# Kernel tuning notes

Measured on AMD Instinct MI355X. Metric: run time of the kernel, lower is better.

The kernel has to match this reference:

```python
import jax, jax.numpy as jnp
import numpy as np
import math

B, H, W, CV = 8, 128, 128, 256
T, CT = 77, 512
HEADS, HEAD_DIM = 8, 32
TOP_M = 5
LN_EPS = 1e-5
NORM_EPS = 1e-6
CLAMP = 2.0


def _ln(x, w, b):
    mu = jnp.mean(x, axis=-1, keepdims=True)
    var = jnp.mean(jnp.square(x - mu), axis=-1, keepdims=True)
    return (x - mu) * jax.lax.rsqrt(var + LN_EPS) * w + b


def _l2norm(x):
    n = jnp.sqrt(jnp.sum(jnp.square(x), axis=-1, keepdims=True))
    return x / jnp.maximum(n, NORM_EPS)


def setup_inputs() -> dict:
    key = jax.random.key(0)
    ks = jax.random.split(key, 12)
    s = 0.02
    return {
        "visual_features": jax.random.normal(ks[0], (B, H, W, CV), jnp.float32),
        "text_features": jax.random.normal(ks[1], (B, T, CT), jnp.float32),
        "norm1_w": jnp.ones((CV,), jnp.float32),
        "norm1_b": jnp.zeros((CV,), jnp.float32),
        "q_w": s * jax.random.normal(ks[2], (CV, CV), jnp.float32),
        "q_b": jnp.zeros((CV,), jnp.float32),
        "k_w": s * jax.random.normal(ks[3], (CT, CV), jnp.float32),
        "k_b": jnp.zeros((CV,), jnp.float32),
        "v_w": s * jax.random.normal(ks[4], (CT, CV), jnp.float32),
        "v_b": jnp.zeros((CV,), jnp.float32),
        "out_w": s * jax.random.normal(ks[5], (CV, CV), jnp.float32),
        "out_b": jnp.zeros((CV,), jnp.float32),
        "gate_w": s * jax.random.normal(ks[6], (CV, 1), jnp.float32),
        "gate_b": jnp.zeros((1,), jnp.float32),
        "logit_scale": jnp.asarray(math.log(1.0 / 0.07), jnp.float32),
        "alpha": jnp.asarray(0.1, jnp.float32),
        "norm2_w": jnp.ones((CV,), jnp.float32),
        "norm2_b": jnp.zeros((CV,), jnp.float32),
        "ffn1_w": s * jax.random.normal(ks[7], (CV, 4 * CV), jnp.float32),
        "ffn1_b": jnp.zeros((4 * CV,), jnp.float32),
        "ffn2_w": s * jax.random.normal(ks[8], (4 * CV, CV), jnp.float32),
        "ffn2_b": jnp.zeros((CV,), jnp.float32),
    }


def reference(visual_features, text_features, norm1_w, norm1_b, q_w, q_b, k_w, k_b,
              v_w, v_b, out_w, out_b, gate_w, gate_b, logit_scale, alpha,
              norm2_w, norm2_b, ffn1_w, ffn1_b, ffn2_w, ffn2_b):
    b, h, w, cv = visual_features.shape
    n = h * w
    # Pre-LN then flatten spatial dims: (B, N, Cv)
    x = _ln(visual_features, norm1_w, norm1_b).reshape(b, n, cv)
    q_full = x @ q_w + q_b                      # (B, N, Cv)
    k_full = text_features @ k_w + k_b          # (B, T, Cv)
    v_full = text_features @ v_w + v_b          # (B, T, Cv)
    # padding mask: all-zero text tokens
    pad = jnp.sum(jnp.abs(text_features), axis=-1) <= 1e-6  # (B, T)
    # cosine-normalize over FULL Cv dim, then split heads
    q = _l2norm(q_full).reshape(b, n, HEADS, HEAD_DIM)
    k = _l2norm(k_full).reshape(b, -1, HEADS, HEAD_DIM)
    v = v_full.reshape(b, -1, HEADS, HEAD_DIM)
    scale = jnp.exp(jnp.clip(logit_scale, -CLAMP, CLAMP)) / jnp.sqrt(jnp.float32(HEAD_DIM))
    sim = jnp.einsum('bnhd,bthd->bnht', q, k) * scale  # (B, N, Hh, T)
    sim = jnp.where(pad[:, None, None, :], -jnp.inf, sim)
    # top-k pruning over text tokens (threshold at k-th value; ties measure-zero)
    topv = jax.lax.top_k(sim, TOP_M)[0]
    sim = jnp.where(sim >= topv[..., -1:], sim, -jnp.inf)
    attn = jax.nn.softmax(sim, axis=-1)
    aligned = jnp.einsum('bnht,bthd->bnhd', attn, v).reshape(b, n, cv)
    aligned = aligned @ out_w + out_b
    gate = jax.nn.sigmoid(x @ gate_w + gate_b)  # (B, N, 1)
    y = x + alpha * gate * aligned
    y = _ln(y, norm2_w, norm2_b)
    ffn = jax.nn.gelu(y @ ffn1_w + ffn1_b, approximate=False) @ ffn2_w + ffn2_b
    y = y + ffn
    return y.reshape(b, h, w, cv)
```

## Files before the change

### kernel.cpp

```cpp
#include <hip/hip_runtime.h>
#include <hip/hip_bf16.h>

typedef _Float16 h16;
typedef __attribute__((ext_vector_type(8))) _Float16 halfx8;
typedef __attribute__((ext_vector_type(4))) _Float16 halfx4;
typedef __attribute__((ext_vector_type(4))) float f32x4;

__device__ __forceinline__ void gload_lds16(const void* g, void* l) {
  __builtin_amdgcn_global_load_lds((const __attribute__((address_space(1))) unsigned int*)g,
                                   (__attribute__((address_space(3))) unsigned int*)l, 16, 0, 0);
}
__device__ __forceinline__ unsigned umax_(unsigned a, unsigned b) { return a > b ? a : b; }
__device__ __forceinline__ unsigned umin_(unsigned a, unsigned b) { return a < b ? a : b; }

__device__ __forceinline__ float fast_gelu(float v) {
  float x2 = v * v;
  float w_ = v * fmaf(x2, 0.0713548163f, 1.5957691216f);
  float e = __expf(w_);
  float r = 1.f / (1.f + e);
  return v * e * r;
}

__global__ __launch_bounds__(256) void conv_all_kernel(
    const float* __restrict__ qw, const float* __restrict__ ow,
    const float* __restrict__ f1w, const float* __restrict__ f2w,
    h16* __restrict__ qwT, h16* __restrict__ owT,
    h16* __restrict__ f1T, h16* __restrict__ f2T)
{
  int bid = blockIdx.x, tid = threadIdx.x;
  const float* in; h16* out; int logN, K, base;
  if (bid < 256)       { in = qw;  out = qwT; logN = 8;  K = 256;  base = 0; }
  else if (bid < 512)  { in = ow;  out = owT; logN = 8;  K = 256;  base = 256; }
  else if (bid < 1536) { in = f1w; out = f1T; logN = 10; K = 256;  base = 512; }
  else                 { in = f2w; out = f2T; logN = 8;  K = 1024; base = 1536; }
  int idx = (bid - base) * 256 + tid;
  int k = idx >> logN, n = idx & ((1 << logN) - 1);
  out[(size_t)n * K + k] = (h16)in[idx];
}

__global__ __launch_bounds__(256) void text_kv_kernel(const float* __restrict__ tf,
    const float* __restrict__ kw, const float* __restrict__ kb,
    const float* __restrict__ vw, const float* __restrict__ vb,
    const float* __restrict__ lsp,
    h16* __restrict__ ko, h16* __restrict__ vo, float* __restrict__ padf)
{
  __shared__ h16 st[4 * 512];
  __shared__ float kro[4 * 256];
  __shared__ float ssc[4];
  int bx = blockIdx.x, b = bx / 20, tg = bx % 20, t0 = tg * 4;
  int tid = threadIdx.x, lane = tid & 63, wid = tid >> 6;
  for (int i = tid; i < 4 * 512; i += 256) {
    int tl = i >> 9, j = i & 511, t = t0 + tl;
    float v = (t < 77) ? tf[((size_t)b * 77 + t) * 512 + j] : 0.f;
    st[i] = (h16)v;
  }
  __syncthreads();
  {
    int t = t0 + wid;
    float a = 0.f;
    #pragma unroll
    for (int j = 0; j < 8; j++) a += fabsf((float)st[wid * 512 + lane + j * 64]);
    #pragma unroll
    for (int o = 32; o; o >>= 1) a += __shfl_xor(a, o);
    if (lane == 0) padf[b * 80 + t] = (a <= 1e-6f) ? -1e30f : 0.f;
  }
  int c = tid;
  float kacc[4], vacc[4];
  #pragma unroll
  for (int tl = 0; tl < 4; tl++) { kacc[tl] = kb[c]; vacc[tl] = vb[c]; }
  for (int j = 0; j < 512; j++) {
    float wkv = kw[(size_t)j * 256 + c];
    float wvv = vw[(size_t)j * 256 + c];
    #pragma unroll
    for (int tl = 0; tl < 4; tl++) {
      float x = (float)st[tl * 512 + j];
      kacc[tl] += x * wkv; vacc[tl] += x * wvv;
    }
  }
  #pragma unroll
  for (int tl = 0; tl < 4; tl++) kro[tl * 256 + c] = kacc[tl] * kacc[tl];
  __syncthreads();
  {
    float s2 = kro[wid * 256 + lane] + kro[wid * 256 + lane + 64]
             + kro[wid * 256 + lane + 128] + kro[wid * 256 + lane + 192];
    #pragma unroll
    for (int o = 32; o; o >>= 1) s2 += __shfl_xor(s2, o);
    if (lane == 0) {
      float ls = lsp[0];
      float scale = __expf(fminf(fmaxf(ls, -2.f), 2.f)) * rsqrtf(32.f);
      ssc[wid] = scale / fmaxf(sqrtf(s2), 1e-6f);
    }
  }
  __syncthreads();
  int h = c >> 5, d = c & 31, g = d >> 3, e = d & 7;
  #pragma unroll
  for (int tl = 0; tl < 4; tl++) {
    int t = t0 + tl;
    int kt = t >> 4, l15 = t & 15, ln = g * 16 + l15;
    size_t koff = ((((size_t)(b * 8 + h) * 5 + kt) * 64) + ln) * 8 + e;
    size_t voff = (((size_t)(b * 8 + h) * 80) + t) * 32 + d;
    ko[koff] = (t < 77) ? (h16)(kacc[tl] * ssc[tl]) : (h16)0.f;
    vo[voff] = (t < 77) ? (h16)vacc[tl] : (h16)0.f;
  }
}

__global__ __launch_bounds__(256) void ln1_kernel(const float* __restrict__ vis,
    const float* __restrict__ w, const float* __restrict__ bia,
    const float* __restrict__ gw, const float* __restrict__ gb,
    h16* __restrict__ x, float* __restrict__ gate)
{
  int lane = threadIdx.x & 63;
  size_t row = (size_t)blockIdx.x * 4 + (threadIdx.x >> 6);
  const float4 v = ((const float4*)(vis + row * 256))[lane];
  float s = v.x + v.y + v.z + v.w;
  float q = v.x * v.x + v.y * v.y + v.z * v.z + v.w * v.w;
  #pragma unroll
  for (int o = 32; o; o >>= 1) { s += __shfl_xor(s, o); q += __shfl_xor(q, o); }
  float mean = s * (1.f / 256.f);
  float rstd = rsqrtf(q * (1.f / 256.f) - mean * mean + 1e-5f);
  float4 wv = ((const float4*)w)[lane], bv = ((const float4*)bia)[lane];
  float x0 = (v.x - mean) * rstd * wv.x + bv.x;
  float x1 = (v.y - mean) * rstd * wv.y + bv.y;
  float x2 = (v.z - mean) * rstd * wv.z + bv.z;
  float x3 = (v.w - mean) * rstd * wv.w + bv.w;
  float4 gv = ((const float4*)gw)[lane];
  float g = x0 * gv.x + x1 * gv.y + x2 * gv.z + x3 * gv.w;
  #pragma unroll
  for (int o = 32; o; o >>= 1) g += __shfl_xor(g, o);
  if (lane == 0) gate[row] = 1.f / (1.f + __expf(-(g + gb[0])));
  halfx4 o4; o4[0] = (h16)x0; o4[1] = (h16)x1; o4[2] = (h16)x2; o4[3] = (h16)x3;
  ((halfx4*)(x + row * 256))[lane] = o4;
}

__global__ __launch_bounds__(256) void gemmQA_kernel(const h16* __restrict__ A,
    const h16* __restrict__ Wt, const float* __restrict__ bias,
    const h16* __restrict__ kk,
    const h16* __restrict__ vv,
    const float* __restrict__ padf,
    h16* __restrict__ outp)
{
  __shared__ char sA[8192];
  __shared__ char sB[32768];
  int m0 = blockIdx.x * 64;
  int tid = threadIdx.x, lane = tid & 63, wid = tid >> 6;
  int wn = wid;
  int l15 = lane & 15, l4 = lane >> 4, xk = l15 & 7;
  f32x4 acc[4][4];
  #pragma unroll
  for (int a = 0; a < 4; a++)
    #pragma unroll
    for (int b2 = 0; b2 < 4; b2++) acc[a][b2] = (f32x4){0.f, 0.f, 0.f, 0.f};
  const size_t sa = 512;
  int srow = lane >> 3;
  int scol = ((lane & 7) ^ srow) * 16;
  const char* Ab = (const char*)A + (size_t)m0 * sa + scol;
  const char* Bb = (const char*)Wt + scol;
  for (int k0 = 0; k0 < 256; k0 += 64) {
    #pragma unroll
    for (int cc = 0; cc < 2; cc++) {
      int ch = wid * 2 + cc;
      gload_lds16(Ab + (size_t)(ch * 8 + srow) * sa + k0 * 2, sA + ch * 1024);
    }
    #pragma unroll
    for (int cc = 0; cc < 8; cc++) {
      int ch = wid * 8 + cc;
      gload_lds16(Bb + (size_t)(ch * 8 + srow) * sa + k0 * 2, sB + ch * 1024);
    }
    asm volatile("s_waitcnt vmcnt(0)" ::: "memory");
    __syncthreads();
    #pragma unroll
    for (int ks = 0; ks < 2; ks++) {
      halfx8 af[4], bf[4];
      #pragma unroll
      for (int f = 0; f < 4; f++) {
        af[f] = *(const halfx8*)(sA + (f * 16 + l15) * 128 + (((ks * 4 + l4) ^ xk) * 16));
        bf[f] = *(const halfx8*)(sB + (wn * 64 + f * 16 + l15) * 128 + (((ks * 4 + l4) ^ xk) * 16));
      }
      #pragma unroll
      for (int fm = 0; fm < 4; fm++)
        #pragma unroll
        for (int fn = 0; fn < 4; fn++)
          acc[fm][fn] = __builtin_amdgcn_mfma_f32_16x16x32_f16(af[fm], bf[fn], acc[fm][fn], 0, 0, 0);
    }
    __syncthreads();
  }
  float bv[4];
  #pragma unroll
  for (int fn = 0; fn < 4; fn++) bv[fn] = bias[wn * 64 + fn * 16 + l15];
  float ps[4][4];
  #pragma unroll
  for (int fm = 0; fm < 4; fm++)
    #pragma unroll
    for (int r = 0; r < 4; r++) {
      float s = 0.f;
      #pragma unroll
      for (int fn = 0; fn < 4; fn++) {
        float v = acc[fm][fn][r] + bv[fn];
        acc[fm][fn][r] = v;
        s += v * v;
      }
      ps[fm][r] = s;
    }
  #pragma unroll
  for (int o = 1; o <= 8; o <<= 1)
    #pragma unroll
    for (int fm = 0; fm < 4; fm++)
      #pragma unroll
      for (int r = 0; r < 4; r++) ps[fm][r] += __shfl_xor(ps[fm][r], o);
  if (l15 == 0) {
    #pragma unroll
    for (int fm = 0; fm < 4; fm++)
      #pragma unroll
      for (int r = 0; r < 4; r++)
        ((float*)sA)[(fm * 16 + l4 * 4 + r) * 4 + wn] = ps[fm][r];
  }
  __syncthreads();
  #pragma unroll
  for (int fm = 0; fm < 4; fm++)
    #pragma unroll
    for (int r = 0; r < 4; r++) {
      const float* p = (const float*)sA + (fm * 16 + l4 * 4 + r) * 4;
      float S = p[0] + p[1] + p[2] + p[3];
      float sc = 1.f / fmaxf(sqrtf(S), 1e-6f);
      int row = fm * 16 + l4 * 4 + r;
      #pragma unroll
      for (int fn = 0; fn < 4; fn++) {
        int col = wn * 64 + fn * 16 + l15;
        ((h16*)(sB + row * 512 + (((col >> 3) ^ (row & 7)) * 16)))[col & 7] =
            (h16)(acc[fm][fn][r] * sc);
      }
    }
  __syncthreads();

  {
    int bx = blockIdx.x;
    int g = l4;
    int b = bx >> 8;
    size_t qrow = (size_t)bx * 64 + wid * 16 + l15;
    int base4 = g * 4;
    float pad4[5][4];
    #pragma unroll
    for (int kt = 0; kt < 5; kt++) {
      float4 p4 = *(const float4*)&padf[b * 80 + kt * 16 + base4];
      pad4[kt][0] = p4.x; pad4[kt][1] = p4.y; pad4[kt][2] = p4.z; pad4[kt][3] = p4.w;
    }
    const char* qsrc = sB + (wid * 16 + l15) * 512;
    int rk = l15 & 7;
    h16* op = &outp[qrow * 256 + g * 8];
    #pragma unroll 2
    for (int h = 0; h < 8; h++) {
      int ho = h * 32;
      halfx8 qf = *(const halfx8*)(qsrc + (((h * 4 + l4) ^ rk) * 16));
      const h16* kph = kk + (((size_t)(b * 8 + h) * 5) * 64 + lane) * 8;
      const h16* vph = vv + ((size_t)(b * 8 + h) * 80) * 32 + g * 8;
      f32x4 acc5[5];
      #pragma unroll
      for (int kt = 0; kt < 5; kt++) {
        halfx8 kf = *(const halfx8*)(kph + kt * 512);
        acc5[kt] = __builtin_amdgcn_mfma_f32_16x16x32_f16(kf, qf, (f32x4){0.f, 0.f, 0.f, 0.f}, 0, 0, 0);
      }
      unsigned pv0 = 0u, pv1 = 0u, pv2 = 0u, pv3 = 0u, pv4 = 0u;
      #pragma unroll
      for (int kt = 0; kt < 5; kt++) {
        #pragma unroll
        for (int r = 0; r < 4; r++) {
          float s = acc5[kt][r] + pad4[kt][r];
          int bi = __float_as_int(s);
          unsigned u = ((unsigned)(bi ^ ((bi >> 31) | (int)0x80000000)) & 0xFFFFFF80u)
                     | (unsigned)(base4 + kt * 16 + r);
          unsigned a;
          a = umax_(pv0, u); u = umin_(pv0, u); pv0 = a;
          a = umax_(pv1, u); u = umin_(pv1, u); pv1 = a;
          a = umax_(pv2, u); u = umin_(pv2, u); pv2 = a;
          a = umax_(pv3, u); u = umin_(pv3, u); pv3 = a;
          pv4 = umax_(pv4, u);
        }
      }
      #pragma unroll
      for (int mrd = 0; mrd < 2; mrd++) {
        int msk = mrd ? 32 : 16;
        unsigned b0 = (unsigned)__shfl_xor((int)pv0, msk);
        unsigned b1 = (unsigned)__shfl_xor((int)pv1, msk);
        unsigned b2 = (unsigned)__shfl_xor((int)pv2, msk);
        unsigned b3 = (unsigned)__shfl_xor((int)pv3, msk);
        unsigned b4 = (unsigned)__shfl_xor((int)pv4, msk);
        unsigned c0 = umax_(pv0, b0);
        unsigned c1 = umax_(umax_(umin_(pv0, b0), pv1), b1);
        unsigned c2 = umax_(umax_(umin_(pv0, b1), umin_(pv1, b0)), umax_(pv2, b2));
        unsigned c3 = umax_(umax_(umax_(umin_(pv0, b2), umin_(pv1, b1)), umin_(pv2, b0)), umax_(pv3, b3));
        unsigned c4 = umax_(umax_(umax_(umin_(pv0, b3), umin_(pv1, b2)),
                                  umax_(umin_(pv2, b1), umin_(pv3, b0))), umax_(pv4, b4));
        pv0 = c0; pv1 = c1; pv2 = c2; pv3 = c3; pv4 = c4;
      }
      unsigned pvs[5] = {pv0, pv1, pv2, pv3, pv4};
      float pw[5]; int ti[5]; float den = 0.f;
      #pragma unroll
      for (int k = 0; k < 5; k++) {
        unsigned u = pvs[k];
        int sg = ((int)u) >> 31;
        float tv = __int_as_float(u ^ (0x80000000u | (unsigned)~sg));
        ti[k] = (int)(u & 0x7Fu);
        pw[k] = __expf(tv);
        den += pw[k];
      }
      float inv = 1.f / den;
      halfx8 o8 = {};
      #pragma unroll
      for (int k = 0; k < 5; k++) {
        h16 ph = (h16)(pw[k] * inv);
        halfx8 v = *(const halfx8*)(vph + ti[k] * 32);
        halfx8 p8 = {ph, ph, ph, ph, ph, ph, ph, ph};
        o8 = o8 + p8 * v;
      }
      *(halfx8*)(op + ho) = o8;
    }
  }
}

__global__ __launch_bounds__(256) void gemmO_kernel(const h16* __restrict__ A,
    const h16* __restrict__ Wt, const float* __restrict__ ob,
    const h16* __restrict__ x, const float* __restrict__ gate,
    const float* __restrict__ alphap, const float* __restrict__ w2,
    const float* __restrict__ b2, h16* __restrict__ outp)
{
  __shared__ char sA[8192];
  __shared__ char sB[32768];
  int m0 = blockIdx.x * 64;
  int tid = threadIdx.x, lane = tid & 63, wid = tid >> 6;
  int wn = wid;
  int l15 = lane & 15, l4 = lane >> 4, xk = l15 & 7;
  f32x4 acc[4][4];
  #pragma unroll
  for (int a = 0; a < 4; a++)
    #pragma unroll
    for (int b2_ = 0; b2_ < 4; b2_++) acc[a][b2_] = (f32x4){0.f, 0.f, 0.f, 0.f};
  const size_t sa = 512;
  int srow = lane >> 3;
  int scol = ((lane & 7) ^ srow) * 16;
  const char* Ab = (const char*)A + (size_t)m0 * sa + scol;
  const char* Bb = (const char*)Wt + scol;
  for (int k0 = 0; k0 < 256; k0 += 64) {
    #pragma unroll
    for (int cc = 0; cc < 2; cc++) {
      int ch = wid * 2 + cc;
      gload_lds16(Ab + (size_t)(ch * 8 + srow) * sa + k0 * 2, sA + ch * 1024);
    }
    #pragma unroll
    for (int cc = 0; cc < 8; cc++) {
      int ch = wid * 8 + cc;
      gload_lds16(Bb + (size_t)(ch * 8 + srow) * sa + k0 * 2, sB + ch * 1024);
    }
    asm volatile("s_waitcnt vmcnt(0)" ::: "memory");
    __syncthreads();
    #pragma unroll
    for (int ks = 0; ks < 2; ks++) {
      halfx8 af[4], bf[4];
      #pragma unroll
      for (int f = 0; f < 4; f++) {
        af[f] = *(const halfx8*)(sA + (f * 16 + l15) * 128 + (((ks * 4 + l4) ^ xk) * 16));
        bf[f] = *(const halfx8*)(sB + (wn * 64 + f * 16 + l15) * 128 + (((ks * 4 + l4) ^ xk) * 16));
      }
      #pragma unroll
      for (int fm = 0; fm < 4; fm++)
        #pragma unroll
        for (int fn = 0; fn < 4; fn++)
          acc[fm][fn] = __builtin_amdgcn_mfma_f32_16x16x32_f16(af[fm], bf[fn], acc[fm][fn], 0, 0, 0);
    }
    __syncthreads();
  }
  float bv[4], w2v[4], b2v[4];
  #pragma unroll
  for (int fn = 0; fn < 4; fn++) {
    int col = wn * 64 + fn * 16 + l15;
    bv[fn] = ob[col]; w2v[fn] = w2[col]; b2v[fn] = b2[col];
  }
  float al = alphap[0];
  float s1[4][4], s2[4][4];
  #pragma unroll
  for (int fm = 0; fm < 4; fm++)
    #pragma unroll
    for (int r = 0; r < 4; r++) {
      size_t row = (size_t)(m0 + fm * 16 + l4 * 4 + r);
      float ga = al * gate[row];
      float a1 = 0.f, a2 = 0.f;
      #pragma unroll
      for (int fn = 0; fn < 4; fn++) {
        float v = acc[fm][fn][r] + bv[fn];
        float xv = (float)x[row * 256 + wn * 64 + fn * 16 + l15];
        float y = xv + ga * v;
        acc[fm][fn][r] = y;
        a1 += y; a2 += y * y;
      }
      s1[fm][r] = a1; s2[fm][r] = a2;
    }
  #pragma unroll
  for (int o = 1; o <= 8; o <<= 1)
    #pragma unroll
    for (int fm = 0; fm < 4; fm++)
      #pragma unroll
      for (int r = 0; r < 4; r++) {
        s1[fm][r] += __shfl_xor(s1[fm][r], o);
        s2[fm][r] += __shfl_xor(s2[fm][r], o);
      }
  if (l15 == 0) {
    #pragma unroll
    for (int fm = 0; fm < 4; fm++)
      #pragma unroll
      for (int r = 0; r < 4; r++) {
        int rr = fm * 16 + l4 * 4 + r;
        ((float*)sA)[rr * 8 + wn * 2 + 0] = s1[fm][r];
        ((float*)sA)[rr * 8 + wn * 2 + 1] = s2[fm][r];
      }
  }
  __syncthreads();
  #pragma unroll
  for (int fm = 0; fm < 4; fm++)
    #pragma unroll
    for (int r = 0; r < 4; r++) {
      int rr = fm * 16 + l4 * 4 + r;
      const float* p = (const float*)sA + rr * 8;
      float S1 = p[0] + p[2] + p[4] + p[6];
      float S2 = p[1] + p[3] + p[5] + p[7];
      float mean = S1 * (1.f / 256.f);
      float var = S2 * (1.f / 256.f) - mean * mean;
      float rstd = rsqrtf(var + 1e-5f);
      size_t row = (size_t)(m0 + rr);
      #pragma unroll
      for (int fn = 0; fn < 4; fn++) {
        float y = acc[fm][fn][r];
        outp[row * 256 + wn * 64 + fn * 16 + l15] =
            (h16)((y - mean) * rstd * w2v[fn] + b2v[fn]);
      }
    }
}

__device__ __forceinline__ void ffn_stage_w1(const h16* __restrict__ w1t,
                                             int c, char* dW1, int tid, int wid)
{
  #pragma unroll
  for (int j = 0; j < 4; j++) {
    int i = j * 512 + tid;
    int r = i >> 5, g = i & 31;
    gload_lds16(w1t + (size_t)(c * 64 + r) * 256 + ((g ^ (r & 7)) * 8),
                dW1 + (j * 512 + wid * 64) * 16);
  }
}
__device__ __forceinline__ void ffn_stage_w2(const h16* __restrict__ w2t,
                                             int c, char* dW2, int tid, int wid)
{
  #pragma unroll
  for (int j = 0; j < 4; j++) {
    int i = j * 512 + tid;
    int r = i >> 3, g = i & 7;
    gload_lds16(w2t + (size_t)r * 1024 + c * 64 + ((g ^ (r & 7)) * 8),
                dW2 + (j * 512 + wid * 64) * 16);
  }
}

__global__ __launch_bounds__(512, 2) void ffn_fused_kernel(
    const h16* __restrict__ y2g, const h16* __restrict__ w1t, const float* __restrict__ b1,
    const h16* __restrict__ w2t, const float* __restrict__ b2, float* __restrict__ outp)
{
  __shared__ char smem[163840];
  float* sE = (float*)smem;

  int m0 = blockIdx.x * 128;
  int tid = threadIdx.x, lane = tid & 63, wid = tid >> 6;
  int l15 = lane & 15, l4 = lane >> 4;
  int wm1 = wid >> 1, wn1 = wid & 1;
  int wm2 = wid >> 2, wn2 = wid & 3;

  halfx8 afy[2][8];
  #pragma unroll
  for (int fm = 0; fm < 2; fm++) {
    size_t row = (size_t)(m0 + wm1 * 32 + fm * 16 + l15);
    #pragma unroll
    for (int ks = 0; ks < 8; ks++)
      afy[fm][ks] = *(const halfx8*)&y2g[row * 256 + ks * 32 + l4 * 8];
  }

  f32x4 acc2[4][4];
  #pragma unroll
  for (int a = 0; a < 4; a++)
    #pragma unroll
    for (int b_ = 0; b_ < 4; b_++) acc2[a][b_] = (f32x4){0.f, 0.f, 0.f, 0.f};

  ffn_stage_w1(w1t, 0, smem, tid, wid);
  float b1v0 = b1[wn1 * 32 + l15];
  float b1v1 = b1[wn1 * 32 + 16 + l15];
  asm volatile("s_waitcnt vmcnt(0)" ::: "memory");
  __builtin_amdgcn_s_barrier();
  asm volatile("" ::: "memory");

  for (int c = 0; c < 16; c++) {
    int buf = c & 1;
    char* sW1c = smem + buf * 32768;
    if (c < 15) ffn_stage_w1(w1t, c + 1, smem + (buf ^ 1) * 32768, tid, wid);
    ffn_stage_w2(w2t, c, smem + 65536 + buf * 32768, tid, wid);
    float nb0 = 0.f, nb1 = 0.f;
    if (c < 15) {
      nb0 = b1[(c + 1) * 64 + wn1 * 32 + l15];
      nb1 = b1[(c + 1) * 64 + wn1 * 32 + 16 + l15];
    }

    f32x4 a1[2][2];
    #pragma unroll
    for (int a = 0; a < 2; a++)
      #pragma unroll
      for (int b_ = 0; b_ < 2; b_++) a1[a][b_] = (f32x4){0.f, 0.f, 0.f, 0.f};
    __builtin_amdgcn_s_setprio(1);
    #pragma unroll
    for (int ks = 0; ks < 8; ks++) {
      #pragma unroll
      for (int fc = 0; fc < 2; fc++) {
        int nrow = wn1 * 32 + fc * 16 + l15;
        halfx8 bf = *(const halfx8*)(sW1c + (size_t)nrow * 512 + (((ks * 4 + l4) ^ (nrow & 7)) * 16));
        #pragma unroll
        for (int fm = 0; fm < 2; fm++)
          a1[fm][fc] = __builtin_amdgcn_mfma_f32_16x16x32_f16(afy[fm][ks], bf, a1[fm][fc], 0, 0, 0);
      }
    }
    __builtin_amdgcn_s_setprio(0);

    {
      char* sHc = smem + 131072 + buf * 16384;
      #pragma unroll
      for (int fm = 0; fm < 2; fm++)
        #pragma unroll
        for (int fc = 0; fc < 2; fc++)
          #pragma unroll
          for (int r = 0; r < 4; r++) {
            int row = wm1 * 32 + fm * 16 + l4 * 4 + r;
            int col = wn1 * 32 + fc * 16 + l15;
            float v = fast_gelu(a1[fm][fc][r] + (fc ? b1v1 : b1v0));
            ((h16*)(sHc + row * 128 + (((col >> 3) ^ (row & 7)) * 16)))[col & 7] = (h16)v;
          }
    }

    if (c > 0) {
      char* sHp = smem + 131072 + (buf ^ 1) * 16384;
      char* sW2p = smem + 65536 + (buf ^ 1) * 32768;
      __builtin_amdgcn_s_setprio(1);
      #pragma unroll
      for (int ks = 0; ks < 2; ks++) {
        halfx8 ah[4], bw[4];
        #pragma unroll
        for (int f = 0; f < 4; f++) {
          int hrow = wm2 * 64 + f * 16 + l15;
          ah[f] = *(const halfx8*)(sHp + hrow * 128 + (((ks * 4 + l4) ^ (hrow & 7)) * 16));
          int wrow = wn2 * 64 + f * 16 + l15;
          bw[f] = *(const halfx8*)(sW2p + (size_t)wrow * 128 + (((ks * 4 + l4) ^ (wrow & 7)) * 16));
        }
        #pragma unroll
        for (int fm = 0; fm < 4; fm++)
          #pragma unroll
          for (int fn = 0; fn < 4; fn++)
            acc2[fm][fn] = __builtin_amdgcn_mfma_f32_16x16x32_f16(ah[fm], bw[fn], acc2[fm][fn], 0, 0, 0);
      }
      __builtin_amdgcn_s_setprio(0);
    }

    asm volatile("s_waitcnt lgkmcnt(0)" ::: "memory");
    asm volatile("s_waitcnt vmcnt(0)" ::: "memory");
    __builtin_amdgcn_s_barrier();
    asm volatile("" ::: "memory");
    b1v0 = nb0; b1v1 = nb1;
  }

  {
    char* sHp = smem + 131072 + 16384;
    char* sW2p = smem + 65536 + 32768;
    __builtin_amdgcn_s_setprio(1);
    #pragma unroll
    for (int ks = 0; ks < 2; ks++) {
      halfx8 ah[4], bw[4];
      #pragma unroll
      for (int f = 0; f < 4; f++) {
        int hrow = wm2 * 64 + f * 16 + l15;
        ah[f] = *(const halfx8*)(sHp + hrow * 128 + (((ks * 4 + l4) ^ (hrow & 7)) * 16));
        int wrow = wn2 * 64 + f * 16 + l15;
        bw[f] = *(const halfx8*)(sW2p + (size_t)wrow * 128 + (((ks * 4 + l4) ^ (wrow & 7)) * 16));
      }
      #pragma unroll
      for (int fm = 0; fm < 4; fm++)
        #pragma unroll
        for (int fn = 0; fn < 4; fn++)
          acc2[fm][fn] = __builtin_amdgcn_mfma_f32_16x16x32_f16(ah[fm], bw[fn], acc2[fm][fn], 0, 0, 0);
    }
    __builtin_amdgcn_s_setprio(0);
  }

  int rowl = tid >> 3, cg = tid & 7;
  #pragma unroll
  for (int half = 0; half < 2; half++) {
    if (wm2 == half) {
      #pragma unroll
      for (int fm = 0; fm < 4; fm++)
        #pragma unroll
        for (int fn = 0; fn < 4; fn++)
          #pragma unroll
          for (int r = 0; r < 4; r++)
            sE[(fm * 16 + l4 * 4 + r) * 264 + wn2 * 64 + fn * 16 + l15] = acc2[fm][fn][r];
    }
    __syncthreads();
    size_t grow = (size_t)(m0 + half * 64 + rowl);
    #pragma unroll
    for (int k = 0; k < 8; k++) {
      int c0 = cg * 4 + k * 32;
      float4 v = *(float4*)&sE[rowl * 264 + c0];
      halfx4 rv = *(const halfx4*)&y2g[grow * 256 + c0];
      float4 bb = *(const float4*)&b2[c0];
      float4 o;
      o.x = v.x + (float)rv[0] + bb.x;
      o.y = v.y + (float)rv[1] + bb.y;
      o.z = v.z + (float)rv[2] + bb.z;
      o.w = v.w + (float)rv[3] + bb.w;
      *(float4*)&outp[grow * 256 + c0] = o;
    }
    __syncthreads();
  }
}

extern "C" void kernel_launch(void* const* d_in, const int* in_sizes, int n_in,
                              void* d_out, int out_size, void* d_ws, size_t ws_size,
                              hipStream_t stream)
{
  const float* vis = (const float*)d_in[0];
  const float* tf  = (const float*)d_in[1];
  const float* n1w = (const float*)d_in[2];
  const float* n1b = (const float*)d_in[3];
  const float* qw  = (const float*)d_in[4];
  const float* qb  = (const float*)d_in[5];
  const float* kw  = (const float*)d_in[6];
  const float* kb  = (const float*)d_in[7];
  const float* vw  = (const float*)d_in[8];
  const float* vb  = (const float*)d_in[9];
  const float* ow  = (const float*)d_in[10];
  const float* ob  = (const float*)d_in[11];
  const float* gw  = (const float*)d_in[12];
  const float* gb  = (const float*)d_in[13];
  const float* ls  = (const float*)d_in[14];
  const float* al  = (const float*)d_in[15];
  const float* n2w = (const float*)d_in[16];
  const float* n2b = (const float*)d_in[17];
  const float* f1w = (const float*)d_in[18];
  const float* f1b = (const float*)d_in[19];
  const float* f2w = (const float*)d_in[20];
  const float* f2b = (const float*)d_in[21];

  char* ws = (char*)d_ws;
  const size_t MB_ = 1024ull * 1024ull;
  h16*  kS   = (h16*)(ws + 0 * MB_);
  h16*  vS   = (h16*)(ws + 1 * MB_);
  float* padf = (float*)(ws + 2 * MB_);
  float* gate = (float*)(ws + 3 * MB_);
  h16*  qwT  = (h16*)(ws + 4 * MB_);
  h16*  owT  = (h16*)(ws + 5 * MB_);
  h16*  f1T  = (h16*)(ws + 6 * MB_);
  h16*  f2T  = (h16*)(ws + 7 * MB_);
  h16*  xh   = (h16*)(ws + 16 * MB_);
  h16*  qh   = (h16*)(ws + 80 * MB_);
  h16*  alg  = (h16*)(ws + 144 * MB_);

  conv_all_kernel<<<2560, 256, 0, stream>>>(qw, ow, f1w, f2w, qwT, owT, f1T, f2T);

  text_kv_kernel<<<160, 256, 0, stream>>>(tf, kw, kb, vw, vb, ls, kS, vS, padf);
  ln1_kernel<<<32768, 256, 0, stream>>>(vis, n1w, n1b, gw, gb, xh, gate);

  gemmQA_kernel<<<2048, 256, 0, stream>>>(xh, qwT, qb, kS, vS, padf, qh);

  gemmO_kernel<<<2048, 256, 0, stream>>>(qh, owT, ob, xh, gate, al, n2w, n2b, alg);

  ffn_fused_kernel<<<1024, 512, 0, stream>>>(alg, f1T, f1b, f2T, f2b, (float*)d_out);
}
```

Measured before the change: 523.9 us.

## Fuse attention output projection, gated residual and LN2 into QA kernel

Merges the Q-GEMM/attention kernel with the output-projection kernel. Each wave keeps its 16 rows of attention output in registers as MFMA A-fragments and multiplies them against the out-projection weights streamed through LDS. The gated residual and second LayerNorm are then applied in-register, so the intermediate aligned tensor is never written to or read back from global memory. The cost is higher register pressure (16 accumulators plus 8 halfx8 held across the loop) and a fully unrolled head loop, which may lower occupancy.

Result: slower. 536.1 us (+2.3%).

```diff
diff --git a/kernel.cpp b/kernel.cpp
--- a/kernel.cpp
+++ b/kernel.cpp
@@ -132,12 +132,16 @@
   ((halfx4*)(x + row * 256))[lane] = o4;
 }
 
-__global__ __launch_bounds__(256) void gemmQA_kernel(const h16* __restrict__ A,
+__global__ __launch_bounds__(256) void gemmQAO_kernel(const h16* __restrict__ A,
     const h16* __restrict__ Wt, const float* __restrict__ bias,
     const h16* __restrict__ kk,
     const h16* __restrict__ vv,
     const float* __restrict__ padf,
-    h16* __restrict__ outp)
+    const h16* __restrict__ Ot,
+    const float* __restrict__ ob,
+    const h16* __restrict__ x, const float* __restrict__ gate,
+    const float* __restrict__ alphap, const float* __restrict__ w2,
+    const float* __restrict__ b2, h16* __restrict__ outp)
 {
   __shared__ char sA[8192];
   __shared__ char sB[32768];
@@ -149,7 +153,7 @@
   #pragma unroll
   for (int a = 0; a < 4; a++)
     #pragma unroll
-    for (int b2 = 0; b2 < 4; b2++) acc[a][b2] = (f32x4){0.f, 0.f, 0.f, 0.f};
+    for (int b2_ = 0; b2_ < 4; b2_++) acc[a][b2_] = (f32x4){0.f, 0.f, 0.f, 0.f};
   const size_t sa = 512;
   int srow = lane >> 3;
   int scol = ((lane & 7) ^ srow) * 16;
@@ -232,12 +236,10 @@
     }
   __syncthreads();
 
+  halfx8 o8s[8];
   {
-    int bx = blockIdx.x;
-    int g = l4;
-    int b = bx >> 8;
-    size_t qrow = (size_t)bx * 64 + wid * 16 + l15;
-    int base4 = g * 4;
+    int b = blockIdx.x >> 8;
+    int base4 = l4 * 4;
     float pad4[5][4];
     #pragma unroll
     for (int kt = 0; kt < 5; kt++) {
@@ -246,13 +248,11 @@
     }
     const char* qsrc = sB + (wid * 16 + l15) * 512;
     int rk = l15 & 7;
-    h16* op = &outp[qrow * 256 + g * 8];
-    #pragma unroll 2
+    #pragma unroll
     for (int h = 0; h < 8; h++) {
-      int ho = h * 32;
       halfx8 qf = *(const halfx8*)(qsrc + (((h * 4 + l4) ^ rk) * 16));
       const h16* kph = kk + (((size_t)(b * 8 + h) * 5) * 64 + lane) * 8;
-      const h16* vph = vv + ((size_t)(b * 8 + h) * 80) * 32 + g * 8;
+      const h16* vph = vv + ((size_t)(b * 8 + h) * 80) * 32 + l4 * 8;
       f32x4 acc5[5];
       #pragma unroll
       for (int kt = 0; kt < 5; kt++) {
@@ -281,14 +281,14 @@
         int msk = mrd ? 32 : 16;
         unsigned b0 = (unsigned)__shfl_xor((int)pv0, msk);
         unsigned b1 = (unsigned)__shfl_xor((int)pv1, msk);
-        unsigned b2 = (unsigned)__shfl_xor((int)pv2, msk);
+        unsigned b2_ = (unsigned)__shfl_xor((int)pv2, msk);
         unsigned b3 = (unsigned)__shfl_xor((int)pv3, msk);
         unsigned b4 = (unsigned)__shfl_xor((int)pv4, msk);
         unsigned c0 = umax_(pv0, b0);
         unsigned c1 = umax_(umax_(umin_(pv0, b0), pv1), b1);
-        unsigned c2 = umax_(umax_(umin_(pv0, b1), umin_(pv1, b0)), umax_(pv2, b2));
-        unsigned c3 = umax_(umax_(umax_(umin_(pv0, b2), umin_(pv1, b1)), umin_(pv2, b0)), umax_(pv3, b3));
-        unsigned c4 = umax_(umax_(umax_(umin_(pv0, b3), umin_(pv1, b2)),
+        unsigned c2 = umax_(umax_(umin_(pv0, b1), umin_(pv1, b0)), umax_(pv2, b2_));
+        unsigned c3 = umax_(umax_(umax_(umin_(pv0, b2_), umin_(pv1, b1)), umin_(pv2, b0)), umax_(pv3, b3));
+        unsigned c4 = umax_(umax_(umax_(umin_(pv0, b3), umin_(pv1, b2_)),
                                   umax_(umin_(pv2, b1), umin_(pv3, b0))), umax_(pv4, b4));
         pv0 = c0; pv1 = c1; pv2 = c2; pv3 = c3; pv4 = c4;
       }
@@ -312,126 +312,87 @@
         halfx8 p8 = {ph, ph, ph, ph, ph, ph, ph, ph};
         o8 = o8 + p8 * v;
       }
-      *(halfx8*)(op + ho) = o8;
-    }
-  }
-}
-
-__global__ __launch_bounds__(256) void gemmO_kernel(const h16* __restrict__ A,
-    const h16* __restrict__ Wt, const float* __restrict__ ob,
-    const h16* __restrict__ x, const float* __restrict__ gate,
-    const float* __restrict__ alphap, const float* __restrict__ w2,
-    const float* __restrict__ b2, h16* __restrict__ outp)
-{
-  __shared__ char sA[8192];
-  __shared__ char sB[32768];
-  int m0 = blockIdx.x * 64;
-  int tid = threadIdx.x, lane = tid & 63, wid = tid >> 6;
-  int wn = wid;
-  int l15 = lane & 15, l4 = lane >> 4, xk = l15 & 7;
-  f32x4 acc[4][4];
-  #pragma unroll
-  for (int a = 0; a < 4; a++)
-    #pragma unroll
-    for (int b2_ = 0; b2_ < 4; b2_++) acc[a][b2_] = (f32x4){0.f, 0.f, 0.f, 0.f};
-  const size_t sa = 512;
-  int srow = lane >> 3;
-  int scol = ((lane & 7) ^ srow) * 16;
-  const char* Ab = (const char*)A + (size_t)m0 * sa + scol;
-  const char* Bb = (const char*)Wt + scol;
+      o8s[h] = o8;
+    }
+  }
+
+  asm volatile("" ::: "memory");
+  __builtin_amdgcn_s_barrier();
+  asm volatile("" ::: "memory");
+
+  f32x4 acc2[16];
+  #pragma unroll
+  for (int fn = 0; fn < 16; fn++) acc2[fn] = (f32x4){0.f, 0.f, 0.f, 0.f};
+  const char* Ob = (const char*)Ot + scol;
   for (int k0 = 0; k0 < 256; k0 += 64) {
-    #pragma unroll
-    for (int cc = 0; cc < 2; cc++) {
-      int ch = wid * 2 + cc;
-      gload_lds16(Ab + (size_t)(ch * 8 + srow) * sa + k0 * 2, sA + ch * 1024);
-    }
     #pragma unroll
     for (int cc = 0; cc < 8; cc++) {
       int ch = wid * 8 + cc;
-      gload_lds16(Bb + (size_t)(ch * 8 + srow) * sa + k0 * 2, sB + ch * 1024);
+      gload_lds16(Ob + (size_t)(ch * 8 + srow) * sa + k0 * 2, sB + ch * 1024);
     }
     asm volatile("s_waitcnt vmcnt(0)" ::: "memory");
-    __syncthreads();
+    __builtin_amdgcn_s_barrier();
+    asm volatile("" ::: "memory");
     #pragma unroll
     for (int ks = 0; ks < 2; ks++) {
-      halfx8 af[4], bf[4];
-      #pragma unroll
-      for (int f = 0; f < 4; f++) {
-        af[f] = *(const halfx8*)(sA + (f * 16 + l15) * 128 + (((ks * 4 + l4) ^ xk) * 16));
-        bf[f] = *(const halfx8*)(sB + (wn * 64 + f * 16 + l15) * 128 + (((ks * 4 + l4) ^ xk) * 16));
-      }
-      #pragma unroll
-      for (int fm = 0; fm < 4; fm++)
-        #pragma unroll
-        for (int fn = 0; fn < 4; fn++)
-          acc[fm][fn] = __builtin_amdgcn_mfma_f32_16x16x32_f16(af[fm], bf[fn], acc[fm][fn], 0, 0, 0);
-    }
-    __syncthreads();
-  }
-  float bv[4], w2v[4], b2v[4];
-  #pragma unroll
-  for (int fn = 0; fn < 4; fn++) {
-    int col = wn * 64 + fn * 16 + l15;
-    bv[fn] = ob[col]; w2v[fn] = w2[col]; b2v[fn] = b2[col];
-  }
-  float al = alphap[0];
-  float s1[4][4], s2[4][4];
-  #pragma unroll
-  for (int fm = 0; fm < 4; fm++)
+      halfx8 af = o8s[(k0 >> 5) + ks];
+      #pragma unroll
+      for (int fn = 0; fn < 16; fn++) {
+        int nrow = fn * 16 + l15;
+        halfx8 bf = *(const halfx8*)(sB + nrow * 128 + (((ks * 4 + l4) ^ (nrow & 7)) * 16));
+        acc2[fn] = __builtin_amdgcn_mfma_f32_16x16x32_f16(af, bf, acc2[fn], 0, 0, 0);
+      }
+    }
+    asm volatile("s_waitcnt lgkmcnt(0)" ::: "memory");
+    __builtin_amdgcn_s_barrier();
+    asm volatile("" ::: "memory");
+  }
+
+  {
+    float al = alphap[0];
+    size_t rbase = (size_t)(m0 + wid * 16 + l4 * 4);
+    float ga4[4];
+    #pragma unroll
+    for (int r = 0; r < 4; r++) ga4[r] = al * gate[rbase + r];
+    float s1[4] = {0.f, 0.f, 0.f, 0.f}, s2[4] = {0.f, 0.f, 0.f, 0.f};
+    #pragma unroll
+    for (int fn = 0; fn < 16; fn++) {
+      int col = fn * 16 + l15;
+      float obc = ob[col];
+      const h16* xp = &x[rbase * 256 + col];
+      #pragma unroll
+      for (int r = 0; r < 4; r++) {
+        float v = acc2[fn][r] + obc;
+        float xv = (float)xp[(size_t)r * 256];
+        float yy = xv + ga4[r] * v;
+        acc2[fn][r] = yy;
+        s1[r] += yy; s2[r] += yy * yy;
+      }
+    }
+    #pragma unroll
+    for (int o = 1; o <= 8; o <<= 1)
+      #pragma unroll
+      for (int r = 0; r < 4; r++) {
+        s1[r] += __shfl_xor(s1[r], o);
+        s2[r] += __shfl_xor(s2[r], o);
+      }
+    float mean[4], rstd[4];
     #pragma unroll
     for (int r = 0; r < 4; r++) {
-      size_t row = (size_t)(m0 + fm * 16 + l4 * 4 + r);
-      float ga = al * gate[row];
-      float a1 = 0.f, a2 = 0.f;
-      #pragma unroll
-      for (int fn = 0; fn < 4; fn++) {
-        float v = acc[fm][fn][r] + bv[fn];
-        float xv = (float)x[row * 256 + wn * 64 + fn * 16 + l15];
-        float y = xv + ga * v;
-        acc[fm][fn][r] = y;
-        a1 += y; a2 += y * y;
-      }
-      s1[fm][r] = a1; s2[fm][r] = a2;
-    }
-  #pragma unroll
-  for (int o = 1; o <= 8; o <<= 1)
-    #pragma unroll
-    for (int fm = 0; fm < 4; fm++)
-      #pragma unroll
-      for (int r = 0; r < 4; r++) {
-        s1[fm][r] += __shfl_xor(s1[fm][r], o);
-        s2[fm][r] += __shfl_xor(s2[fm][r], o);
-      }
-  if (l15 == 0) {
-    #pragma unroll
-    for (int fm = 0; fm < 4; fm++)
-      #pragma unroll
-      for (int r = 0; r < 4; r++) {
-        int rr = fm * 16 + l4 * 4 + r;
-        ((float*)sA)[rr * 8 + wn * 2 + 0] = s1[fm][r];
-        ((float*)sA)[rr * 8 + wn * 2 + 1] = s2[fm][r];
-      }
-  }
-  __syncthreads();
-  #pragma unroll
-  for (int fm = 0; fm < 4; fm++)
-    #pragma unroll
-    for (int r = 0; r < 4; r++) {
-      int rr = fm * 16 + l4 * 4 + r;
-      const float* p = (const float*)sA + rr * 8;
-      float S1 = p[0] + p[2] + p[4] + p[6];
-      float S2 = p[1] + p[3] + p[5] + p[7];
-      float mean = S1 * (1.f / 256.f);
-      float var = S2 * (1.f / 256.f) - mean * mean;
-      float rstd = rsqrtf(var + 1e-5f);
-      size_t row = (size_t)(m0 + rr);
-      #pragma unroll
-      for (int fn = 0; fn < 4; fn++) {
-        float y = acc[fm][fn][r];
-        outp[row * 256 + wn * 64 + fn * 16 + l15] =
-            (h16)((y - mean) * rstd * w2v[fn] + b2v[fn]);
-      }
-    }
+      mean[r] = s1[r] * (1.f / 256.f);
+      float var = s2[r] * (1.f / 256.f) - mean[r] * mean[r];
+      rstd[r] = rsqrtf(var + 1e-5f);
+    }
+    #pragma unroll
+    for (int fn = 0; fn < 16; fn++) {
+      int col = fn * 16 + l15;
+      float wc = w2[col], bc = b2[col];
+      h16* op2 = &outp[rbase * 256 + col];
+      #pragma unroll
+      for (int r = 0; r < 4; r++)
+        op2[(size_t)r * 256] = (h16)((acc2[fn][r] - mean[r]) * rstd[r] * wc + bc);
+    }
+  }
 }
 
 __device__ __forceinline__ void ffn_stage_w1(const h16* __restrict__ w1t,
@@ -659,7 +620,6 @@
   h16*  f1T  = (h16*)(ws + 6 * MB_);
   h16*  f2T  = (h16*)(ws + 7 * MB_);
   h16*  xh   = (h16*)(ws + 16 * MB_);
-  h16*  qh   = (h16*)(ws + 80 * MB_);
   h16*  alg  = (h16*)(ws + 144 * MB_);
 
   conv_all_kernel<<<2560, 256, 0, stream>>>(qw, ow, f1w, f2w, qwT, owT, f1T, f2T);
@@ -667,9 +627,8 @@
   text_kv_kernel<<<160, 256, 0, stream>>>(tf, kw, kb, vw, vb, ls, kS, vS, padf);
   ln1_kernel<<<32768, 256, 0, stream>>>(vis, n1w, n1b, gw, gb, xh, gate);
 
-  gemmQA_kernel<<<2048, 256, 0, stream>>>(xh, qwT, qb, kS, vS, padf, qh);
-
-  gemmO_kernel<<<2048, 256, 0, stream>>>(qh, owT, ob, xh, gate, al, n2w, n2b, alg);
+  gemmQAO_kernel<<<2048, 256, 0, stream>>>(xh, qwT, qb, kS, vS, padf,
+                                           owT, ob, xh, gate, al, n2w, n2b, alg);
 
   ffn_fused_kernel<<<1024, 512, 0, stream>>>(alg, f1T, f1b, f2T, f2b, (float*)d_out);
 }
```
